# Kernel optimization log

Measured on AMD Instinct MI355X. Metric: run time of the kernel, lower is better.

## Reference

```python
import jax, jax.numpy as jnp
import numpy as np

T, D_IN, D_OUT, L, R = 8192, 4096, 4096, 16, 16


def setup_inputs() -> dict:
    key = jax.random.key(0)
    ks = jax.random.split(key, 7)
    x = jax.random.normal(ks[0], (T, D_IN), dtype=jnp.float32)
    W = jax.random.normal(ks[1], (D_OUT, D_IN), dtype=jnp.float32) / np.sqrt(D_IN)
    base_bias = jax.random.normal(ks[2], (D_OUT,), dtype=jnp.float32)
    # stacked LoRA weights (squeezed over the dummy dim-1 in the torch code)
    lora_a = jax.random.normal(ks[3], (L, R, D_IN), dtype=jnp.float32) / np.sqrt(D_IN)
    lora_b = jax.random.normal(ks[4], (L, D_OUT, R), dtype=jnp.float32) / np.sqrt(R)
    bias_stacked = jax.random.normal(ks[5], (L, D_OUT), dtype=jnp.float32)
    # per-token adapter index in [-1, L); -1 means "no LoRA"
    indices = jax.random.randint(ks[6], (T,), -1, L, dtype=jnp.int32)
    return {"x": x, "W": W, "base_bias": base_bias, "lora_a": lora_a,
            "lora_b": lora_b, "bias_stacked": bias_stacked, "indices": indices}


def reference(x, W, base_bias, lora_a, lora_b, bias_stacked, indices):
    num_loras = lora_a.shape[0]
    # base dense GEMM + base bias (ReplicatedLinear.quant_method.apply)
    out = x @ W.T + base_bias  # [T, D_OUT]
    # one_hot gives an all-zero row for indices == -1, matching the masking
    # in apply_bias and the no-op semantics of add_lora for unmapped tokens.
    onehot = jax.nn.one_hot(indices, num_loras, dtype=x.dtype)  # [T, L]
    # per-adapter bias gather-scatter (apply_bias)
    out = out + onehot @ bias_stacked  # [T, D_OUT]
    # SGMV-style LoRA: shrink with A, expand with B, scatter-add into out.
    shrunk_all = jnp.einsum('td,lrd->ltr', x, lora_a)        # [L, T, R]
    shrunk = jnp.einsum('tl,ltr->tr', onehot, shrunk_all)    # [T, R] per-token
    masked = onehot[:, :, None] * shrunk[:, None, :]         # [T, L, R]
    out = out + jnp.einsum('tlr,lor->to', masked, lora_b)    # [T, D_OUT]
    return out
```

## Files before the change

### kernel.cpp

```cpp
#include <hip/hip_runtime.h>
#include <hip/hip_bf16.h>
#include <stdint.h>

typedef unsigned short u16;
typedef unsigned int u32;

#define T_TOK 8192
#define DIN   4096
#define DOUT  4096
#define NL    16
#define NR    16
#define KX    4096
#define K2    4416
#define NKT   69
#define GITERS 34

typedef __attribute__((ext_vector_type(8))) __bf16 bf16x8;
typedef __attribute__((ext_vector_type(4))) float  f32x4;

__device__ __forceinline__ u32 bf16rne(float f) {
    u32 x = __float_as_uint(f);
    return (x + 0x7FFFu + ((x >> 16) & 1u)) >> 16;
}
__device__ __forceinline__ u32 pack2(float a, float b) {
    return bf16rne(a) | (bf16rne(b) << 16);
}
__device__ __forceinline__ float bf2f(u32 u) {
    return __uint_as_float(u << 16);
}
__device__ __forceinline__ void unpack8(uint4 v, float* f) {
    f[0] = bf2f(v.x & 0xFFFFu); f[1] = bf2f(v.x >> 16);
    f[2] = bf2f(v.y & 0xFFFFu); f[3] = bf2f(v.y >> 16);
    f[4] = bf2f(v.z & 0xFFFFu); f[5] = bf2f(v.z >> 16);
    f[6] = bf2f(v.w & 0xFFFFu); f[7] = bf2f(v.w >> 16);
}


__global__ void pack_mat(const float* __restrict__ src, u16* __restrict__ dst, int rows) {
    const int total = rows * (DIN / 8);
    for (int i = blockIdx.x * blockDim.x + threadIdx.x; i < total;
         i += gridDim.x * blockDim.x) {
        int row = i >> 9;
        int c8  = (i & 511) << 3;
        const float4* s = (const float4*)(src + (size_t)row * DIN + c8);
        float4 f0 = s[0], f1 = s[1];
        uint4 u;
        u.x = pack2(f0.x, f0.y); u.y = pack2(f0.z, f0.w);
        u.z = pack2(f1.x, f1.y); u.w = pack2(f1.z, f1.w);
        *(uint4*)(dst + (size_t)row * K2 + c8) = u;
    }
}

__global__ void pack_bextra(const float* __restrict__ lora_b,
                            const float* __restrict__ base_bias,
                            const float* __restrict__ bias_st,
                            u16* __restrict__ Bbf) {
    const int total = DOUT * 320;
    for (int i = blockIdx.x * blockDim.x + threadIdx.x; i < total;
         i += gridDim.x * blockDim.x) {
        int o = i / 320;
        int j = i - o * 320;
        float v = 0.f;
        if (j < 256) {
            int l = j >> 4, r = j & 15;
            v = lora_b[((size_t)l * DOUT + o) * NR + r];
        } else if (j == 256) {
            v = base_bias[o];
        } else if (j < 273) {
            v = bias_st[(size_t)(j - 257) * DOUT + o];
        }
        Bbf[(size_t)o * K2 + KX + j] = (u16)bf16rne(v);
    }
}

__global__ void conv_la(const float* __restrict__ la, u16* __restrict__ dst) {
    const int total = NL * NR * DIN / 8;
    for (int i = blockIdx.x * blockDim.x + threadIdx.x; i < total;
         i += gridDim.x * blockDim.x) {
        int c8 = i << 3;
        const float4* s = (const float4*)(la + c8);
        float4 f0 = s[0], f1 = s[1];
        uint4 u;
        u.x = pack2(f0.x, f0.y); u.y = pack2(f0.z, f0.w);
        u.z = pack2(f1.x, f1.y); u.w = pack2(f1.z, f1.w);
        *(uint4*)(dst + c8) = u;
    }
}

__global__ __launch_bounds__(256) void shrink_kernel(const int* __restrict__ idx,
                                                     const u16* __restrict__ Aabf,
                                                     u16* __restrict__ Abf) {
    int wid  = threadIdx.x >> 6;
    int lane = threadIdx.x & 63;
    int t = blockIdx.x * 4 + wid;
    int l = idx[t];

    u16* rowp = Abf + (size_t)t * K2;
    u32* z = (u32*)(rowp + KX);

    float acc[16];
#pragma unroll
    for (int r = 0; r < 16; ++r) acc[r] = 0.f;

    if (l >= 0) {
        const u16* xr = rowp;
        const u16* ab = Aabf + (size_t)l * (NR * DIN);
#pragma unroll
        for (int c = 0; c < 8; ++c) {
            uint4 xv = *(const uint4*)(xr + c * 512 + lane * 8);
            float xf[8];
            unpack8(xv, xf);
#pragma unroll
            for (int r = 0; r < 16; ++r) {
                uint4 av = *(const uint4*)(ab + r * DIN + c * 512 + lane * 8);
                float af[8];
                unpack8(av, af);
#pragma unroll
                for (int e = 0; e < 8; ++e) acc[r] = fmaf(xf[e], af[e], acc[r]);
            }
        }
#pragma unroll
        for (int s = 1; s < 64; s <<= 1) {
#pragma unroll
            for (int r = 0; r < 16; ++r) acc[r] += __shfl_xor(acc[r], s, 64);
        }
    }

#pragma unroll
    for (int q = 0; q < 2; ++q) {
        int j = lane + q * 64;
        bool isval = (l >= 0) && (j >= l * 8) && (j < l * 8 + 8);
        if (!isval) z[j] = 0u;
    }
    if (lane < 32) {
        int e0 = KX + 256 + 2 * lane;
        u32 v0 = (e0 == 4352 || (l >= 0 && e0 == 4353 + l)) ? 0x3F80u : 0u;
        int e1 = e0 + 1;
        u32 v1 = (e1 == 4352 || (l >= 0 && e1 == 4353 + l)) ? 0x3F80u : 0u;
        z[128 + lane] = v0 | (v1 << 16);
    }
    if (l >= 0 && lane == 0) {
        u32* zp = z + l * 8;
#pragma unroll
        for (int j = 0; j < 8; ++j) zp[j] = pack2(acc[2 * j], acc[2 * j + 1]);
    }
}


#define SBAR() __builtin_amdgcn_sched_barrier(0)
#define HWBAR() __builtin_amdgcn_s_barrier()
#define PHASE_BAR() do { SBAR(); HWBAR(); SBAR(); } while (0)
#define VMCNT6() asm volatile("s_waitcnt vmcnt(6)" ::: "memory")
#define VMCNT0() asm volatile("s_waitcnt vmcnt(0)" ::: "memory")

#define STAGE(ptr, h, buf, seg, kt)                                                   \
  do { if ((kt) < NKT) {                                                              \
    __builtin_amdgcn_global_load_lds(                                                 \
      (const __attribute__((address_space(1))) u32*)((ptr) + (size_t)((h)*128 + 0)*K2 + (size_t)(kt)*64),  \
      (__attribute__((address_space(3))) u32*)(lds16 + ((((buf)*4+(seg))<<13) + tid*8)), 16, 0, 0);        \
    __builtin_amdgcn_global_load_lds(                                                 \
      (const __attribute__((address_space(1))) u32*)((ptr) + (size_t)((h)*128 + 64)*K2 + (size_t)(kt)*64), \
      (__attribute__((address_space(3))) u32*)(lds16 + ((((buf)*4+(seg))<<13) + tid*8 + 4096)), 16, 0, 0); \
  } } while (0)

#define RD_A(buf)                                                                     \
  { _Pragma("unroll") for (int m = 0; m < 8; ++m)                                     \
    _Pragma("unroll") for (int kk = 0; kk < 2; ++kk)                                  \
      a[m][kk] = *(const bf16x8*)(smem + (((buf)*4 + wr) << 14) + lrow*128 + m*2048 + kxb[kk]); }

#define RD_B(buf, nh, bf)                                                             \
  { _Pragma("unroll") for (int nn = 0; nn < 2; ++nn)                                  \
    _Pragma("unroll") for (int kk = 0; kk < 2; ++kk)                                  \
      bf[nn][kk] = *(const bf16x8*)(smem + (((buf)*4 + 2 + (wc>>1)) << 14)            \
          + ((wc&1)*64 + lrow)*128 + ((nh)*2+nn)*2048 + kxb[kk]); }

#define MMQ(mh, nh, bf)                                                               \
  { __builtin_amdgcn_s_setprio(1);                                                    \
    _Pragma("unroll") for (int mm = 0; mm < 4; ++mm)                                  \
    _Pragma("unroll") for (int nn = 0; nn < 2; ++nn)                                  \
    _Pragma("unroll") for (int kk = 0; kk < 2; ++kk)                                  \
      acc[(mh)*4+mm][(nh)*2+nn] = __builtin_amdgcn_mfma_f32_16x16x32_bf16(            \
          a[(mh)*4+mm][kk], bf[nn][kk], acc[(mh)*4+mm][(nh)*2+nn], 0, 0, 0);          \
    __builtin_amdgcn_s_setprio(0); }

__global__ __launch_bounds__(512, 2) void gemm_kernel(const u16* __restrict__ A,
                                                      const u16* __restrict__ B,
                                                      float* __restrict__ C) {
    __shared__ u16 lds16[65536];
    const char* smem = (const char*)lds16;

    const int tid  = threadIdx.x;
    const int lane = tid & 63, wid = tid >> 6;
    const int wr = wid >> 2, wc = wid & 3;
    const int lrow = lane & 15;
    const int klo  = (lane >> 4) << 4;
    const int sx   = (lrow & 7) << 4;
    const int kxb[2] = { klo ^ sx, (64 + klo) ^ sx };

    const int wg  = blockIdx.x;
    const int swz = (wg & 7) * 64 + (wg >> 3);
    const int bm = swz >> 4;
    const int bn = swz & 15;

    const int r0  = tid >> 3;
    const int sc4 = (tid & 7) ^ (r0 & 7);
    const u16* pA = A + (size_t)(bm * 256 + r0) * K2 + sc4 * 8;
    const u16* pB = B + (size_t)(bn * 256 + r0) * K2 + sc4 * 8;

    f32x4 acc[8][4];
#pragma unroll
    for (int m = 0; m < 8; ++m)
#pragma unroll
        for (int n = 0; n < 4; ++n) {
            f32x4 z = {0.f, 0.f, 0.f, 0.f};
            acc[m][n] = z;
        }
    bf16x8 a[8][2], bA[2][2], bB[2][2];

    STAGE(pA, 0, 0, 0, 0); STAGE(pA, 1, 0, 1, 0);
    STAGE(pB, 0, 0, 2, 0); STAGE(pB, 1, 0, 3, 0);
    STAGE(pA, 0, 1, 0, 1); STAGE(pA, 1, 1, 1, 1);
    STAGE(pB, 0, 1, 2, 1);
    VMCNT6();
    PHASE_BAR();

    for (int i = 0; i < GITERS; ++i) {
        const int k1  = 2 * i + 1;
        const int kn  = 2 * i + 2;
        const int kn1 = 2 * i + 3;
        RD_A(0); RD_B(0, 0, bA);
        STAGE(pB, 1, 1, 3, k1);
        PHASE_BAR();
        MMQ(0, 0, bA);
        PHASE_BAR();
        STAGE(pA, 0, 0, 0, kn);
        PHASE_BAR();
        MMQ(1, 0, bA);
        PHASE_BAR();
        RD_B(0, 1, bB);
        STAGE(pA, 1, 0, 1, kn);
        PHASE_BAR();
        MMQ(0, 1, bB);
        PHASE_BAR();
        STAGE(pB, 0, 0, 2, kn);
        PHASE_BAR();
        MMQ(1, 1, bB);
        VMCNT6();
        PHASE_BAR();
        RD_A(1); RD_B(1, 0, bA);
        STAGE(pB, 1, 0, 3, kn);
        PHASE_BAR();
        MMQ(0, 0, bA);
        PHASE_BAR();
        STAGE(pA, 0, 1, 0, kn1);
        PHASE_BAR();
        MMQ(1, 0, bA);
        PHASE_BAR();
        RD_B(1, 1, bB);
        STAGE(pA, 1, 1, 1, kn1);
        PHASE_BAR();
        MMQ(0, 1, bB);
        PHASE_BAR();
        STAGE(pB, 0, 1, 2, kn1);
        PHASE_BAR();
        MMQ(1, 1, bB);
        VMCNT6();
        PHASE_BAR();
    }

    VMCNT0();
    PHASE_BAR();
    RD_A(0); RD_B(0, 0, bA); RD_B(0, 1, bB);
    MMQ(0, 0, bA); MMQ(1, 0, bA); MMQ(0, 1, bB); MMQ(1, 1, bB);

    const int crow0 = bm * 256 + wr * 128 + ((lane >> 4) << 2);
    const int ccol0 = bn * 256 + wc * 64 + (lane & 15);
#pragma unroll
    for (int m = 0; m < 8; ++m)
#pragma unroll
        for (int n = 0; n < 4; ++n)
#pragma unroll
            for (int rg = 0; rg < 4; ++rg)
                C[(size_t)(crow0 + m * 16 + rg) * DOUT + ccol0 + n * 16] = acc[m][n][rg];
}


extern "C" void kernel_launch(void* const* d_in, const int* in_sizes, int n_in,
                              void* d_out, int out_size, void* d_ws, size_t ws_size,
                              hipStream_t stream) {
    const float* x         = (const float*)d_in[0];
    const float* W         = (const float*)d_in[1];
    const float* base_bias = (const float*)d_in[2];
    const float* lora_a    = (const float*)d_in[3];
    const float* lora_b    = (const float*)d_in[4];
    const float* bias_st   = (const float*)d_in[5];
    const int*   indices   = (const int*)d_in[6];
    float* out = (float*)d_out;

    u16* Abf  = (u16*)d_ws;
    u16* Bbf  = Abf + (size_t)T_TOK * K2;
    u16* Aabf = Bbf + (size_t)DOUT * K2;

    pack_mat<<<4096, 256, 0, stream>>>(x, Abf, T_TOK);
    pack_mat<<<2048, 256, 0, stream>>>(W, Bbf, DOUT);
    pack_bextra<<<2048, 256, 0, stream>>>(lora_b, base_bias, bias_st, Bbf);
    conv_la<<<512, 256, 0, stream>>>(lora_a, Aabf);
    shrink_kernel<<<T_TOK / 4, 256, 0, stream>>>(indices, Aabf, Abf);
    gemm_kernel<<<512, 512, 0, stream>>>(Abf, Bbf, out);
    (void)in_sizes; (void)n_in; (void)out_size; (void)ws_size;
}
```

Before: 369.4 us.

## Use MFMA for LoRA shrink, merge pack kernels, and retune GEMM pipeline

The per-token scalar-FMA LoRA shrink kernel is replaced by an MFMA-based kernel. It computes x times all stacked LoRA A rows for 64-token tiles through LDS double buffering, then keeps only the selected adapter's columns. The five prep launches become three: the x and W packing merge into one kernel, and lora_b/bias packing merges with the lora_a conversion. The GEMM main loop now splits the A fragments into two halves loaded just before use, which lowers register pressure, and restages loads with a shallower vmcnt wait. In exchange, the shrink computes all 16 adapters per token, 16x the FLOPs, though on matrix cores, and the GEMM prefetch distance changes.

Measured after the change: 342.5 us. 7.3% less time.

```diff
diff --git a/kernel.cpp b/kernel.cpp
--- a/kernel.cpp
+++ b/kernel.cpp
@@ -25,60 +25,19 @@
 __device__ __forceinline__ u32 pack2(float a, float b) {
     return bf16rne(a) | (bf16rne(b) << 16);
 }
-__device__ __forceinline__ float bf2f(u32 u) {
-    return __uint_as_float(u << 16);
-}
-__device__ __forceinline__ void unpack8(uint4 v, float* f) {
-    f[0] = bf2f(v.x & 0xFFFFu); f[1] = bf2f(v.x >> 16);
-    f[2] = bf2f(v.y & 0xFFFFu); f[3] = bf2f(v.y >> 16);
-    f[4] = bf2f(v.z & 0xFFFFu); f[5] = bf2f(v.z >> 16);
-    f[6] = bf2f(v.w & 0xFFFFu); f[7] = bf2f(v.w >> 16);
-}
-
-
-__global__ void pack_mat(const float* __restrict__ src, u16* __restrict__ dst, int rows) {
-    const int total = rows * (DIN / 8);
+
+__global__ void pack_mats(const float* __restrict__ x, const float* __restrict__ W,
+                          u16* __restrict__ Abf, u16* __restrict__ Bbf) {
+    const int total = (T_TOK + DOUT) * (DIN / 8);
     for (int i = blockIdx.x * blockDim.x + threadIdx.x; i < total;
          i += gridDim.x * blockDim.x) {
         int row = i >> 9;
         int c8  = (i & 511) << 3;
-        const float4* s = (const float4*)(src + (size_t)row * DIN + c8);
-        float4 f0 = s[0], f1 = s[1];
-        uint4 u;
-        u.x = pack2(f0.x, f0.y); u.y = pack2(f0.z, f0.w);
-        u.z = pack2(f1.x, f1.y); u.w = pack2(f1.z, f1.w);
-        *(uint4*)(dst + (size_t)row * K2 + c8) = u;
-    }
-}
-
-__global__ void pack_bextra(const float* __restrict__ lora_b,
-                            const float* __restrict__ base_bias,
-                            const float* __restrict__ bias_st,
-                            u16* __restrict__ Bbf) {
-    const int total = DOUT * 320;
-    for (int i = blockIdx.x * blockDim.x + threadIdx.x; i < total;
-         i += gridDim.x * blockDim.x) {
-        int o = i / 320;
-        int j = i - o * 320;
-        float v = 0.f;
-        if (j < 256) {
-            int l = j >> 4, r = j & 15;
-            v = lora_b[((size_t)l * DOUT + o) * NR + r];
-        } else if (j == 256) {
-            v = base_bias[o];
-        } else if (j < 273) {
-            v = bias_st[(size_t)(j - 257) * DOUT + o];
-        }
-        Bbf[(size_t)o * K2 + KX + j] = (u16)bf16rne(v);
-    }
-}
-
-__global__ void conv_la(const float* __restrict__ la, u16* __restrict__ dst) {
-    const int total = NL * NR * DIN / 8;
-    for (int i = blockIdx.x * blockDim.x + threadIdx.x; i < total;
-         i += gridDim.x * blockDim.x) {
-        int c8 = i << 3;
-        const float4* s = (const float4*)(la + c8);
+        const float* src;
+        u16* dst;
+        if (row < T_TOK) { src = x + (size_t)row * DIN; dst = Abf + (size_t)row * K2; }
+        else { src = W + (size_t)(row - T_TOK) * DIN; dst = Bbf + (size_t)(row - T_TOK) * K2; }
+        const float4* s = (const float4*)(src + c8);
         float4 f0 = s[0], f1 = s[1];
         uint4 u;
         u.x = pack2(f0.x, f0.y); u.y = pack2(f0.z, f0.w);
@@ -87,62 +46,149 @@
     }
 }
 
-__global__ __launch_bounds__(256) void shrink_kernel(const int* __restrict__ idx,
-                                                     const u16* __restrict__ Aabf,
-                                                     u16* __restrict__ Abf) {
-    int wid  = threadIdx.x >> 6;
-    int lane = threadIdx.x & 63;
-    int t = blockIdx.x * 4 + wid;
-    int l = idx[t];
-
-    u16* rowp = Abf + (size_t)t * K2;
-    u32* z = (u32*)(rowp + KX);
-
-    float acc[16];
-#pragma unroll
-    for (int r = 0; r < 16; ++r) acc[r] = 0.f;
-
-    if (l >= 0) {
-        const u16* xr = rowp;
-        const u16* ab = Aabf + (size_t)l * (NR * DIN);
-#pragma unroll
-        for (int c = 0; c < 8; ++c) {
-            uint4 xv = *(const uint4*)(xr + c * 512 + lane * 8);
-            float xf[8];
-            unpack8(xv, xf);
-#pragma unroll
-            for (int r = 0; r < 16; ++r) {
-                uint4 av = *(const uint4*)(ab + r * DIN + c * 512 + lane * 8);
-                float af[8];
-                unpack8(av, af);
-#pragma unroll
-                for (int e = 0; e < 8; ++e) acc[r] = fmaf(xf[e], af[e], acc[r]);
+#define NBEX (DOUT * 320)
+__global__ void pack_small(const float* __restrict__ lora_b,
+                           const float* __restrict__ base_bias,
+                           const float* __restrict__ bias_st,
+                           const float* __restrict__ la,
+                           u16* __restrict__ Bbf, u16* __restrict__ Aabf) {
+    const int total = NBEX + NL * NR * DIN / 8;
+    for (int i = blockIdx.x * blockDim.x + threadIdx.x; i < total;
+         i += gridDim.x * blockDim.x) {
+        if (i < NBEX) {
+            int o = i / 320;
+            int j = i - o * 320;
+            float v = 0.f;
+            if (j < 256) {
+                int l = j >> 4, r = j & 15;
+                v = lora_b[((size_t)l * DOUT + o) * NR + r];
+            } else if (j == 256) {
+                v = base_bias[o];
+            } else if (j < 273) {
+                v = bias_st[(size_t)(j - 257) * DOUT + o];
+            }
+            Bbf[(size_t)o * K2 + KX + j] = (u16)bf16rne(v);
+        } else {
+            int c8 = (i - NBEX) << 3;
+            const float4* s = (const float4*)(la + c8);
+            float4 f0 = s[0], f1 = s[1];
+            uint4 u;
+            u.x = pack2(f0.x, f0.y); u.y = pack2(f0.z, f0.w);
+            u.z = pack2(f1.x, f1.y); u.w = pack2(f1.z, f1.w);
+            *(uint4*)(Aabf + c8) = u;
+        }
+    }
+}
+
+__global__ __launch_bounds__(512) void zfill_kernel(const u16* __restrict__ Axr,
+                                                    const u16* __restrict__ La,
+                                                    const int* __restrict__ idx,
+                                                    u16* __restrict__ Abf) {
+    __shared__ u16 sX[2][64 * 64];
+    __shared__ u16 sL[2][128 * 64];
+    const int tid  = threadIdx.x;
+    const int lane = tid & 63, wid = tid >> 6;
+    const int wr = wid >> 2, wc = wid & 3;
+    const int lrow = lane & 15;
+    const int klo  = (lane >> 4) << 4;
+    const int sxr  = (lrow & 7) << 4;
+    const int kxb[2] = { klo ^ sxr, (64 + klo) ^ sxr };
+
+    const int bt = blockIdx.x >> 1;
+    const int nh = blockIdx.x & 1;
+
+    const int r0 = tid >> 3;
+    const int c4 = (tid & 7) ^ (r0 & 7);
+    const u16* pX = Axr + (size_t)(bt * 64 + r0) * K2 + c4 * 8;
+    const u16* pL = La + (size_t)(nh * 128 + r0) * DIN + c4 * 8;
+    const u16* pL2 = La + (size_t)(nh * 128 + 64 + r0) * DIN + c4 * 8;
+
+    f32x4 acc[2][2];
+#pragma unroll
+    for (int m = 0; m < 2; ++m)
+#pragma unroll
+        for (int n = 0; n < 2; ++n) { f32x4 z = {0.f,0.f,0.f,0.f}; acc[m][n] = z; }
+
+#define STAGEZ(buf, kt)                                                                \
+  do {                                                                                 \
+    __builtin_amdgcn_global_load_lds(                                                  \
+      (const __attribute__((address_space(1))) u32*)(pX + (size_t)(kt) * 64),          \
+      (__attribute__((address_space(3))) u32*)(&sX[buf][tid * 8]), 16, 0, 0);          \
+    __builtin_amdgcn_global_load_lds(                                                  \
+      (const __attribute__((address_space(1))) u32*)(pL + (size_t)(kt) * 64),          \
+      (__attribute__((address_space(3))) u32*)(&sL[buf][tid * 8]), 16, 0, 0);          \
+    __builtin_amdgcn_global_load_lds(                                                  \
+      (const __attribute__((address_space(1))) u32*)(pL2 + (size_t)(kt) * 64),         \
+      (__attribute__((address_space(3))) u32*)(&sL[buf][4096 + tid * 8]), 16, 0, 0);   \
+  } while (0)
+
+    STAGEZ(0, 0);
+    for (int kt = 0; kt < 64; ++kt) {
+        const int cur = kt & 1;
+        if (kt < 63) {
+            STAGEZ(cur ^ 1, kt + 1);
+            asm volatile("s_waitcnt vmcnt(3)" ::: "memory");
+        } else {
+            asm volatile("s_waitcnt vmcnt(0)" ::: "memory");
+        }
+        __builtin_amdgcn_sched_barrier(0);
+        __builtin_amdgcn_s_barrier();
+        __builtin_amdgcn_sched_barrier(0);
+        const char* sx = (const char*)sX[cur];
+        const char* sl = (const char*)sL[cur];
+        bf16x8 a[2][2], b[2][2];
+#pragma unroll
+        for (int m = 0; m < 2; ++m)
+#pragma unroll
+            for (int kk = 0; kk < 2; ++kk)
+                a[m][kk] = *(const bf16x8*)(sx + (wr * 32 + m * 16 + lrow) * 128 + kxb[kk]);
+#pragma unroll
+        for (int n = 0; n < 2; ++n)
+#pragma unroll
+            for (int kk = 0; kk < 2; ++kk)
+                b[n][kk] = *(const bf16x8*)(sl + (wc * 32 + n * 16 + lrow) * 128 + kxb[kk]);
+#pragma unroll
+        for (int m = 0; m < 2; ++m)
+#pragma unroll
+            for (int n = 0; n < 2; ++n)
+#pragma unroll
+                for (int kk = 0; kk < 2; ++kk)
+                    acc[m][n] = __builtin_amdgcn_mfma_f32_16x16x32_bf16(
+                        a[m][kk], b[n][kk], acc[m][n], 0, 0, 0);
+        __builtin_amdgcn_sched_barrier(0);
+        __builtin_amdgcn_s_barrier();
+        __builtin_amdgcn_sched_barrier(0);
+    }
+
+#pragma unroll
+    for (int m = 0; m < 2; ++m) {
+#pragma unroll
+        for (int rg = 0; rg < 4; ++rg) {
+            int tl = wr * 32 + m * 16 + ((lane >> 4) << 2) + rg;
+            int t  = bt * 64 + tl;
+            int l  = idx[t];
+#pragma unroll
+            for (int n = 0; n < 2; ++n) {
+                int col = nh * 128 + wc * 32 + n * 16 + (lane & 15);
+                u16 v = ((col >> 4) == l) ? (u16)bf16rne(acc[m][n][rg]) : (u16)0;
+                Abf[(size_t)t * K2 + KX + col] = v;
             }
         }
-#pragma unroll
-        for (int s = 1; s < 64; s <<= 1) {
-#pragma unroll
-            for (int r = 0; r < 16; ++r) acc[r] += __shfl_xor(acc[r], s, 64);
+    }
+    if (nh == 0) {
+        int tl = tid >> 3, c8 = (tid & 7) * 8;
+        int t = bt * 64 + tl;
+        int l = idx[t];
+        u32 w[4];
+#pragma unroll
+        for (int q = 0; q < 4; ++q) {
+            int c0 = KX + 256 + c8 + 2 * q;
+            u32 v0 = (c0 == 4352 || (l >= 0 && c0 == 4353 + l)) ? 0x3F80u : 0u;
+            int c1 = c0 + 1;
+            u32 v1 = (c1 == 4352 || (l >= 0 && c1 == 4353 + l)) ? 0x3F80u : 0u;
+            w[q] = v0 | (v1 << 16);
         }
-    }
-
-#pragma unroll
-    for (int q = 0; q < 2; ++q) {
-        int j = lane + q * 64;
-        bool isval = (l >= 0) && (j >= l * 8) && (j < l * 8 + 8);
-        if (!isval) z[j] = 0u;
-    }
-    if (lane < 32) {
-        int e0 = KX + 256 + 2 * lane;
-        u32 v0 = (e0 == 4352 || (l >= 0 && e0 == 4353 + l)) ? 0x3F80u : 0u;
-        int e1 = e0 + 1;
-        u32 v1 = (e1 == 4352 || (l >= 0 && e1 == 4353 + l)) ? 0x3F80u : 0u;
-        z[128 + lane] = v0 | (v1 << 16);
-    }
-    if (l >= 0 && lane == 0) {
-        u32* zp = z + l * 8;
-#pragma unroll
-        for (int j = 0; j < 8; ++j) zp[j] = pack2(acc[2 * j], acc[2 * j + 1]);
+        *(uint4*)(Abf + (size_t)t * K2 + KX + 256 + c8) = *(uint4*)w;
     }
 }
 
@@ -150,7 +196,7 @@
 #define SBAR() __builtin_amdgcn_sched_barrier(0)
 #define HWBAR() __builtin_amdgcn_s_barrier()
 #define PHASE_BAR() do { SBAR(); HWBAR(); SBAR(); } while (0)
-#define VMCNT6() asm volatile("s_waitcnt vmcnt(6)" ::: "memory")
+#define VMCNT4() asm volatile("s_waitcnt vmcnt(4)" ::: "memory")
 #define VMCNT0() asm volatile("s_waitcnt vmcnt(0)" ::: "memory")
 
 #define STAGE(ptr, h, buf, seg, kt)                                                   \
@@ -163,24 +209,25 @@
       (__attribute__((address_space(3))) u32*)(lds16 + ((((buf)*4+(seg))<<13) + tid*8 + 4096)), 16, 0, 0); \
   } } while (0)
 
-#define RD_A(buf)                                                                     \
-  { _Pragma("unroll") for (int m = 0; m < 8; ++m)                                     \
+#define RD_AH(buf, mh, aa)                                                            \
+  { _Pragma("unroll") for (int mm = 0; mm < 4; ++mm)                                  \
     _Pragma("unroll") for (int kk = 0; kk < 2; ++kk)                                  \
-      a[m][kk] = *(const bf16x8*)(smem + (((buf)*4 + wr) << 14) + lrow*128 + m*2048 + kxb[kk]); }
-
-#define RD_B(buf, nh, bf)                                                             \
+      aa[mm][kk] = *(const bf16x8*)(smem + (((buf)*4 + wr) << 14) + lrow*128          \
+          + (mh)*8192 + mm*2048 + kxb[kk]); }
+
+#define RD_BH(buf, nh, bf)                                                            \
   { _Pragma("unroll") for (int nn = 0; nn < 2; ++nn)                                  \
     _Pragma("unroll") for (int kk = 0; kk < 2; ++kk)                                  \
       bf[nn][kk] = *(const bf16x8*)(smem + (((buf)*4 + 2 + (wc>>1)) << 14)            \
           + ((wc&1)*64 + lrow)*128 + ((nh)*2+nn)*2048 + kxb[kk]); }
 
-#define MMQ(mh, nh, bf)                                                               \
+#define MMQ(mh, nh, aa, bf)                                                           \
   { __builtin_amdgcn_s_setprio(1);                                                    \
     _Pragma("unroll") for (int mm = 0; mm < 4; ++mm)                                  \
     _Pragma("unroll") for (int nn = 0; nn < 2; ++nn)                                  \
     _Pragma("unroll") for (int kk = 0; kk < 2; ++kk)                                  \
       acc[(mh)*4+mm][(nh)*2+nn] = __builtin_amdgcn_mfma_f32_16x16x32_bf16(            \
-          a[(mh)*4+mm][kk], bf[nn][kk], acc[(mh)*4+mm][(nh)*2+nn], 0, 0, 0);          \
+          aa[mm][kk], bf[nn][kk], acc[(mh)*4+mm][(nh)*2+nn], 0, 0, 0);                \
     __builtin_amdgcn_s_setprio(0); }
 
 __global__ __launch_bounds__(512, 2) void gemm_kernel(const u16* __restrict__ A,
@@ -211,67 +258,63 @@
 #pragma unroll
     for (int m = 0; m < 8; ++m)
 #pragma unroll
-        for (int n = 0; n < 4; ++n) {
-            f32x4 z = {0.f, 0.f, 0.f, 0.f};
-            acc[m][n] = z;
-        }
-    bf16x8 a[8][2], bA[2][2], bB[2][2];
+        for (int n = 0; n < 4; ++n) { f32x4 z = {0.f,0.f,0.f,0.f}; acc[m][n] = z; }
+    bf16x8 a0[4][2], a1[4][2], bA[2][2], bB[2][2];
 
     STAGE(pA, 0, 0, 0, 0); STAGE(pA, 1, 0, 1, 0);
     STAGE(pB, 0, 0, 2, 0); STAGE(pB, 1, 0, 3, 0);
     STAGE(pA, 0, 1, 0, 1); STAGE(pA, 1, 1, 1, 1);
-    STAGE(pB, 0, 1, 2, 1);
-    VMCNT6();
+    VMCNT4();
     PHASE_BAR();
 
     for (int i = 0; i < GITERS; ++i) {
-        const int k1  = 2 * i + 1;
-        const int kn  = 2 * i + 2;
-        const int kn1 = 2 * i + 3;
-        RD_A(0); RD_B(0, 0, bA);
+        const int k1 = 2 * i + 1, kn = 2 * i + 2, kn1 = 2 * i + 3;
+        RD_AH(0, 0, a0); RD_BH(0, 0, bA);
+        STAGE(pB, 0, 1, 2, k1);
+        PHASE_BAR();
+        MMQ(0, 0, a0, bA);
+        PHASE_BAR();
+        RD_AH(0, 1, a1);
         STAGE(pB, 1, 1, 3, k1);
         PHASE_BAR();
-        MMQ(0, 0, bA);
-        PHASE_BAR();
+        MMQ(1, 0, a1, bA);
+        PHASE_BAR();
+        RD_BH(0, 1, bB);
         STAGE(pA, 0, 0, 0, kn);
         PHASE_BAR();
-        MMQ(1, 0, bA);
-        PHASE_BAR();
-        RD_B(0, 1, bB);
+        MMQ(0, 1, a0, bB);
+        PHASE_BAR();
         STAGE(pA, 1, 0, 1, kn);
         PHASE_BAR();
-        MMQ(0, 1, bB);
-        PHASE_BAR();
+        MMQ(1, 1, a1, bB);
+        VMCNT4();
+        PHASE_BAR();
+        RD_AH(1, 0, a0); RD_BH(1, 0, bA);
         STAGE(pB, 0, 0, 2, kn);
         PHASE_BAR();
-        MMQ(1, 1, bB);
-        VMCNT6();
-        PHASE_BAR();
-        RD_A(1); RD_B(1, 0, bA);
+        MMQ(0, 0, a0, bA);
+        PHASE_BAR();
+        RD_AH(1, 1, a1);
         STAGE(pB, 1, 0, 3, kn);
         PHASE_BAR();
-        MMQ(0, 0, bA);
-        PHASE_BAR();
+        MMQ(1, 0, a1, bA);
+        PHASE_BAR();
+        RD_BH(1, 1, bB);
         STAGE(pA, 0, 1, 0, kn1);
         PHASE_BAR();
-        MMQ(1, 0, bA);
-        PHASE_BAR();
-        RD_B(1, 1, bB);
+        MMQ(0, 1, a0, bB);
+        PHASE_BAR();
         STAGE(pA, 1, 1, 1, kn1);
         PHASE_BAR();
-        MMQ(0, 1, bB);
-        PHASE_BAR();
-        STAGE(pB, 0, 1, 2, kn1);
-        PHASE_BAR();
-        MMQ(1, 1, bB);
-        VMCNT6();
+        MMQ(1, 1, a1, bB);
+        VMCNT4();
         PHASE_BAR();
     }
 
     VMCNT0();
     PHASE_BAR();
-    RD_A(0); RD_B(0, 0, bA); RD_B(0, 1, bB);
-    MMQ(0, 0, bA); MMQ(1, 0, bA); MMQ(0, 1, bB); MMQ(1, 1, bB);
+    RD_AH(0, 0, a0); RD_AH(0, 1, a1); RD_BH(0, 0, bA); RD_BH(0, 1, bB);
+    MMQ(0, 0, a0, bA); MMQ(1, 0, a1, bA); MMQ(0, 1, a0, bB); MMQ(1, 1, a1, bB);
 
     const int crow0 = bm * 256 + wr * 128 + ((lane >> 4) << 2);
     const int ccol0 = bn * 256 + wc * 64 + (lane & 15);
@@ -301,11 +344,9 @@
     u16* Bbf  = Abf + (size_t)T_TOK * K2;
     u16* Aabf = Bbf + (size_t)DOUT * K2;
 
-    pack_mat<<<4096, 256, 0, stream>>>(x, Abf, T_TOK);
-    pack_mat<<<2048, 256, 0, stream>>>(W, Bbf, DOUT);
-    pack_bextra<<<2048, 256, 0, stream>>>(lora_b, base_bias, bias_st, Bbf);
-    conv_la<<<512, 256, 0, stream>>>(lora_a, Aabf);
-    shrink_kernel<<<T_TOK / 4, 256, 0, stream>>>(indices, Aabf, Abf);
+    pack_mats<<<6144, 256, 0, stream>>>(x, W, Abf, Bbf);
+    pack_small<<<1536, 256, 0, stream>>>(lora_b, base_bias, bias_st, lora_a, Bbf, Aabf);
+    zfill_kernel<<<256, 512, 0, stream>>>(Abf, Aabf, indices, Abf);
     gemm_kernel<<<512, 512, 0, stream>>>(Abf, Bbf, out);
     (void)in_sizes; (void)n_in; (void)out_size; (void)ws_size;
 }
```
